# Optimization experiments

Hardware: AMD Instinct MI355X
Metric: run time of the kernel (lower is better)

The kernel has to match this reference:

```python
import jax, jax.numpy as jnp
import numpy as np

N_NODES = 100000
N_REL = 8
IN_FEATS = 64
ATTN_FEATS = 32
NUM_HEADS = 4
N_EDGES = 800000
NEG_SLOPE = 0.2


def setup_inputs() -> dict:
    key = jax.random.key(0)
    ks = jax.random.split(key, 11)
    s = 0.05
    return {
        "feat": jax.random.normal(ks[0], (N_NODES, IN_FEATS), jnp.float32),
        "quality_emb": jax.random.normal(ks[1], (N_NODES, IN_FEATS), jnp.float32),
        "fc_src_w": jax.random.normal(ks[2], (N_REL, IN_FEATS, ATTN_FEATS * NUM_HEADS), jnp.float32) * s,
        "fc_src_b": jax.random.normal(ks[3], (N_REL, ATTN_FEATS * NUM_HEADS), jnp.float32) * s,
        "fc_qual_w": jax.random.normal(ks[4], (N_REL, IN_FEATS, ATTN_FEATS * NUM_HEADS), jnp.float32) * s,
        "fc_qual_b": jax.random.normal(ks[5], (N_REL, ATTN_FEATS * NUM_HEADS), jnp.float32) * s,
        "attn": jax.random.normal(ks[6], (N_REL, NUM_HEADS, ATTN_FEATS), jnp.float32) * s,
        "src": jax.random.randint(ks[7], (N_EDGES,), 0, N_NODES, jnp.int64),
        "dst": jax.random.randint(ks[8], (N_EDGES,), 0, N_NODES, jnp.int64),
        "r_type": jax.random.randint(ks[9], (N_EDGES,), 0, N_REL, jnp.int64),
        "nid": jax.random.randint(ks[10], (N_EDGES,), 0, N_NODES, jnp.int64),
    }


def reference(feat, quality_emb, fc_src_w, fc_src_b, fc_qual_w, fc_qual_b, attn,
              src, dst, r_type, nid):
    # gather_mm(feat[src], fc_src_w, idx_b=r_type) == project per node for all
    # relations (grouped GEMM), then gather [src, r_type] per edge.
    feat_proj = jnp.einsum('ni,rio->nro', feat, fc_src_w)          # [N, R, H*D]
    el = feat_proj[src, r_type] + fc_src_b[r_type]                 # [E, H*D]

    qual_proj = jnp.einsum('ni,rio->nro', quality_emb, fc_qual_w)  # [N, R, H*D]
    qual = qual_proj[nid, r_type] + fc_qual_b[r_type]              # [E, H*D]

    e = jax.nn.leaky_relu((el + qual).reshape(-1, NUM_HEADS, ATTN_FEATS), NEG_SLOPE)
    score = jnp.sum(e * attn[r_type], axis=-1)                     # [E, H]

    # edge softmax grouped by destination node, per head
    m = jax.ops.segment_max(score, dst, num_segments=N_NODES)      # [N, H]
    p = jnp.exp(score - m[dst])
    denom = jax.ops.segment_sum(p, dst, num_segments=N_NODES)      # [N, H]
    a = p / denom[dst]                                             # [E, H]

    # narre: messages use raw source features, weighted by attention
    msg = feat[src][:, None, :] * a[:, :, None]                    # [E, H, IN]
    ft = jax.ops.segment_sum(msg, dst, num_segments=N_NODES)       # [N, H, IN]
    return ft
```

## Files before the change

### kernel.cpp

```cpp
#include <hip/hip_runtime.h>
#include <hip/hip_bf16.h>

#define RELS 8
#define HDD 128
#define NH 4
#define STILES 4
#define MAXDEG 64
#define CAP 104448

typedef __attribute__((ext_vector_type(8))) short bf16x8;
typedef __attribute__((ext_vector_type(4))) float f32x4;
typedef unsigned short u16;

__device__ __forceinline__ u16 f2b(float v){
  union { float f; unsigned u; } x; x.f = v;
  unsigned r = x.u + 0x7fffu + ((x.u >> 16) & 1u);
  return (u16)(r >> 16);
}
__device__ __forceinline__ float b2f(u16 h){
  union { unsigned u; float f; } x; x.u = ((unsigned)h) << 16; return x.f;
}

template<int CTRL>
__device__ __forceinline__ float dpp_mov(float x){
  union { float f; int i; } u; u.f = x;
  u.i = __builtin_amdgcn_update_dpp(0, u.i, CTRL, 0xF, 0xF, false);
  return u.f;
}
__device__ __forceinline__ float row_sum16(float v){
  v += dpp_mov<0x121>(v);
  v += dpp_mov<0x122>(v);
  v += dpp_mov<0x124>(v);
  v += dpp_mov<0x128>(v);
  return v;
}

__global__ void k_prep(const float* __restrict__ wsrc, const float* __restrict__ wqual,
                       const float* __restrict__ bsrc, const float* __restrict__ bqual,
                       u16* __restrict__ Wt, float* __restrict__ biasc,
                       const float* __restrict__ feat, const float* __restrict__ qual,
                       u16* __restrict__ featb, u16* __restrict__ qualb, int total,
                       const int* __restrict__ rt, const int* __restrict__ src,
                       const int* __restrict__ nid, const int* __restrict__ dst,
                       int* __restrict__ rcur, int* __restrict__ deg,
                       int* __restrict__ eIdx,
                       int* __restrict__ srcR, int* __restrict__ nidR, int E,
                       int B2, int B0){
  int b = blockIdx.x, t = threadIdx.x;
  if (b < B2){
    __shared__ int lh[RELS], lb[RELS];
    if (t < RELS) lh[t] = 0;
    __syncthreads();
    int e = b*256 + t;
    int r = 0, rank = 0, sv = 0, nv = 0, dv = 0, rk = 0;
    if (e < E){
      dv = dst[e];
      rk = atomicAdd(&deg[dv], 1);
      sv = src[e]; nv = nid[e];
      r = rt[e];
      rank = atomicAdd(&lh[r], 1);
    }
    __syncthreads();
    if (t < RELS && lh[t] > 0) lb[t] = t*CAP + atomicAdd(&rcur[t], lh[t]);
    __syncthreads();
    if (e < E){
      int pr = lb[r] + rank;
      if (pr < (r+1)*CAP){
        srcR[pr] = sv;
        nidR[pr] = nv;
        if (rk < MAXDEG) eIdx[(size_t)dv*MAXDEG + rk] = pr;
      }
    }
  } else if (b < B2 + B0){
    int g = (b - B2)*256 + t;
    if (g < RELS*HDD*HDD){
      int r = g >> 14, rem = g & 16383, n = rem >> 7, k = rem & 127;
      float v = (k < 64) ? wsrc[r*8192 + k*128 + n] : wqual[r*8192 + (k-64)*128 + n];
      Wt[g] = f2b(v);
    } else {
      int bb = g - RELS*HDD*HDD;
      if (bb < RELS*HDD) biasc[bb] = bsrc[bb] + bqual[bb];
    }
  } else {
    int g = ((b - B2 - B0)*256 + t) * 8;
    const float* sp; u16* dp;
    if (g < total){ sp = feat; dp = featb; }
    else { g -= total; if (g >= total) return; sp = qual; dp = qualb; }
    float4 a = *(const float4*)(sp + g);
    float4 c = *(const float4*)(sp + g + 4);
    union { u16 h[8]; uint4 v; } o;
    o.h[0]=f2b(a.x); o.h[1]=f2b(a.y); o.h[2]=f2b(a.z); o.h[3]=f2b(a.w);
    o.h[4]=f2b(c.x); o.h[5]=f2b(c.y); o.h[6]=f2b(c.z); o.h[7]=f2b(c.w);
    *(uint4*)(dp + g) = o.v;
  }
}

__global__ __launch_bounds__(256) void k_score(
    const u16* __restrict__ featb, const u16* __restrict__ qualb,
    const u16* __restrict__ Wt, const float* __restrict__ biasc,
    const float* __restrict__ attn,
    const int* __restrict__ srcR, const int* __restrict__ nidR,
    const int* __restrict__ rcur,
    float* __restrict__ scoreR){
  __shared__ u16 As[2][64*128];
  int t = threadIdx.x;

  const int NBPR = CAP/256;
  int bid = blockIdx.x;
  int r = bid / NBPR, ch = bid - r*NBPR;
  int cnt_r = min(rcur[r], CAP);
  int base = r*CAP + ch*256;
  int cntR = min(256, cnt_r - ch*256);
  if (cntR <= 0) return;
  int Tact = (cntR + 63) >> 6;

  int mloc = t >> 2, part = t & 3;
  int lane = t & 63, w = t >> 6;
  int lr = lane & 15, lq = lane >> 4;

  const u16* wbase = Wt + r*16384 + (w*32)*128;
  bf16x8 wfrag[2][4];
  #pragma unroll
  for (int mt=0; mt<2; mt++)
    #pragma unroll
    for (int kt=0; kt<4; kt++)
      wfrag[mt][kt] = *(const bf16x8*)(wbase + (mt*16 + lr)*128 + kt*32 + lq*8);

  float attn_p[2][4], attn_n[2][4];
  f32x4 biasv[2];
  #pragma unroll
  for (int mt=0; mt<2; mt++)
    #pragma unroll
    for (int i=0; i<4; i++){
      int c = w*32 + mt*16 + lq*4 + i;
      float a = attn[r*128 + c];
      biasv[mt][i] = biasc[r*128 + c];
      attn_p[mt][i] = a;
      attn_n[mt][i] = 0.2f*a;
    }

  const u16* basep = (part < 2) ? featb : qualb;
  int halfoff = (part & 1)*32;
  int myidx[STILES];
  #pragma unroll
  for (int tt=0; tt<STILES; tt++){
    int eloc = tt*64 + mloc;
    int gi = base + eloc;
    myidx[tt] = (eloc < cntR) ? ((part < 2) ? srcR[gi] : nidR[gi]) : -1;
  }

  uint4 pre[2][4];
  auto fetch = [&](int pb, int idxval){
    if (idxval >= 0){
      const uint4* pv = (const uint4*)(basep + (long long)idxval*64 + halfoff);
      pre[pb][0]=pv[0]; pre[pb][1]=pv[1]; pre[pb][2]=pv[2]; pre[pb][3]=pv[3];
    } else {
      uint4 z = {0,0,0,0};
      pre[pb][0]=z; pre[pb][1]=z; pre[pb][2]=z; pre[pb][3]=z;
    }
  };

  fetch(0, myidx[0]);
  fetch(1, myidx[1]);
  #pragma unroll
  for (int tt=0; tt<STILES; tt++){
    if (tt >= Tact) break;
    const int p = tt & 1;
    uint4* As_v = (uint4*)As[p];
    #pragma unroll
    for (int i=0;i<4;i++){
      int c = part*4 + i;
      As_v[mloc*16 + (c ^ part ^ (mloc & 7))] = pre[p][i];
    }
    if (tt+2 < STILES) fetch(p, myidx[tt+2]);
    asm volatile("s_waitcnt lgkmcnt(0)" ::: "memory");
    __builtin_amdgcn_s_barrier();

    f32x4 acc[4][2];
    #pragma unroll
    for (int et=0; et<4; et++){ acc[et][0]=biasv[0]; acc[et][1]=biasv[1]; }
    #pragma unroll
    for (int et=0; et<4; et++){
      #pragma unroll
      for (int kt=0; kt<4; kt++){
        bf16x8 bf = *(const bf16x8*)&As[p][(et*16 + lr)*128 + (((kt*4 + lq) ^ kt ^ (lr & 7))*8)];
        acc[et][0] = __builtin_amdgcn_mfma_f32_16x16x32_bf16(wfrag[0][kt], bf, acc[et][0], 0, 0, 0);
        acc[et][1] = __builtin_amdgcn_mfma_f32_16x16x32_bf16(wfrag[1][kt], bf, acc[et][1], 0, 0, 0);
      }
    }

    float s0v=0.f, s1v=0.f, s2v=0.f, s3v=0.f;
    #pragma unroll
    for (int mt=0; mt<2; mt++)
      #pragma unroll
      for (int i=0; i<4; i++){
        float x0 = acc[0][mt][i];
        s0v = __builtin_fmaf(fmaxf(x0,0.f), attn_p[mt][i], s0v);
        s0v = __builtin_fmaf(fminf(x0,0.f), attn_n[mt][i], s0v);
        float x1 = acc[1][mt][i];
        s1v = __builtin_fmaf(fmaxf(x1,0.f), attn_p[mt][i], s1v);
        s1v = __builtin_fmaf(fminf(x1,0.f), attn_n[mt][i], s1v);
        float x2 = acc[2][mt][i];
        s2v = __builtin_fmaf(fmaxf(x2,0.f), attn_p[mt][i], s2v);
        s2v = __builtin_fmaf(fminf(x2,0.f), attn_n[mt][i], s2v);
        float x3 = acc[3][mt][i];
        s3v = __builtin_fmaf(fmaxf(x3,0.f), attn_p[mt][i], s3v);
        s3v = __builtin_fmaf(fminf(x3,0.f), attn_n[mt][i], s3v);
      }
    s0v += __shfl_xor(s0v, 16); s0v += __shfl_xor(s0v, 32);
    s1v += __shfl_xor(s1v, 16); s1v += __shfl_xor(s1v, 32);
    s2v += __shfl_xor(s2v, 16); s2v += __shfl_xor(s2v, 32);
    s3v += __shfl_xor(s3v, 16); s3v += __shfl_xor(s3v, 32);
    float v01 = (lq & 1) ? s1v : s0v;
    float v23 = (lq & 1) ? s3v : s2v;
    float v = (lq & 2) ? v23 : v01;
    v = __expf(v);
    int eout = tt*64 + lane;
    if (eout < cntR) scoreR[(size_t)(base + eout)*4 + w] = v;
  }
}

__global__ __launch_bounds__(256) void k_agg(
    const int* __restrict__ deg_a, const int* __restrict__ eIdx,
    const float* __restrict__ scoreR, const int* __restrict__ srcR,
    const u16* __restrict__ featb, float* __restrict__ out, int N){
  __shared__ float ps[4][64][4];
  __shared__ int   ss[4][64];
  int wv = threadIdx.x >> 6, lane = threadIdx.x & 63;
  int node = blockIdx.x*4 + wv;
  if (node >= N) return;
  int deg = min(deg_a[node], MAXDEG);
  float a0=0.f, a1=0.f, a2=0.f, a3=0.f;
  if (deg > 0){
    float d0=0.f,d1=0.f,d2=0.f,d3=0.f;
    float p0=0.f,p1=0.f,p2=0.f,p3=0.f; int sv=0;
    if (lane < deg){
      int pr = eIdx[(size_t)node*MAXDEG + lane];
      float4 sc = *(const float4*)&scoreR[(size_t)pr*4];
      sv = srcR[pr];
      p0=sc.x; p1=sc.y; p2=sc.z; p3=sc.w;
    }
    d0=p0; d1=p1; d2=p2; d3=p3;
    float4 pv = { p0, p1, p2, p3 };
    *(float4*)&ps[wv][lane][0] = pv;
    ss[wv][lane] = sv;
    __builtin_amdgcn_wave_barrier();
    #pragma unroll 4
    for (int e=0; e<deg; e++){
      float4 pe = *(const float4*)&ps[wv][e][0];
      float fv = b2f(featb[(long long)ss[wv][e]*64 + lane]);
      a0 += pe.x*fv; a1 += pe.y*fv; a2 += pe.z*fv; a3 += pe.w*fv;
    }
    __builtin_amdgcn_wave_barrier();
    d0=row_sum16(d0); d1=row_sum16(d1); d2=row_sum16(d2); d3=row_sum16(d3);
    #pragma unroll
    for (int off=16; off<64; off<<=1){
      d0+=__shfl_xor(d0,off); d1+=__shfl_xor(d1,off);
      d2+=__shfl_xor(d2,off); d3+=__shfl_xor(d3,off);
    }
    a0 *= 1.f/d0; a1 *= 1.f/d1; a2 *= 1.f/d2; a3 *= 1.f/d3;
  }
  float* op = out + (long long)node*256;
  op[lane]       = a0;
  op[64 + lane]  = a1;
  op[128 + lane] = a2;
  op[192 + lane] = a3;
}

extern "C" void kernel_launch(void* const* d_in, const int* in_sizes, int n_in,
                              void* d_out, int out_size, void* d_ws, size_t ws_size,
                              hipStream_t stream) {
  const float* feat  = (const float*)d_in[0];
  const float* qual  = (const float*)d_in[1];
  const float* wsrc  = (const float*)d_in[2];
  const float* bsrc  = (const float*)d_in[3];
  const float* wqual = (const float*)d_in[4];
  const float* bqual = (const float*)d_in[5];
  const float* attn  = (const float*)d_in[6];
  const int* src = (const int*)d_in[7];
  const int* dst = (const int*)d_in[8];
  const int* rt  = (const int*)d_in[9];
  const int* nid = (const int*)d_in[10];
  const int E = in_sizes[7];
  const int N = in_sizes[0] / 64;
  float* out = (float*)d_out;

  char* p = (char*)d_ws;
  auto alloc = [&](size_t bytes) -> void* {
    void* q = (void*)p;
    p += (bytes + 255) & ~(size_t)255;
    return q;
  };
  float* scoreR  = (float*)alloc((size_t)RELS*CAP*4*4);
  u16*  featb    = (u16*)  alloc((size_t)N*64*2);
  u16*  qualb    = (u16*)  alloc((size_t)N*64*2);
  u16*  Wt       = (u16*)  alloc((size_t)RELS*HDD*HDD*2);
  float* biasc   = (float*)alloc((size_t)RELS*HDD*4);
  int*  srcR     = (int*)  alloc((size_t)RELS*CAP*4);
  int*  nidR     = (int*)  alloc((size_t)RELS*CAP*4);
  int*  eIdx     = (int*)  alloc((size_t)N*MAXDEG*4);
  char* zbase = p;
  int*  deg      = (int*)  alloc((size_t)N*4);
  int*  rcur     = (int*)  alloc(32);
  size_t zbytes = (size_t)(p - zbase);

  hipMemsetAsync(zbase, 0, zbytes, stream);

  int total = N*64;
  int totw = RELS*HDD*HDD + RELS*HDD;
  int B2 = (E + 255)/256;
  int B0 = (totw + 255)/256;
  int B1 = ((2*total)/8 + 255)/256;
  k_prep<<<B2+B0+B1, 256, 0, stream>>>(wsrc, wqual, bsrc, bqual, Wt, biasc,
                                       feat, qual, featb, qualb, total,
                                       rt, src, nid, dst,
                                       rcur, deg, eIdx, srcR, nidR, E, B2, B0);
  k_score<<<RELS*(CAP/256), 256, 0, stream>>>(featb, qualb, Wt, biasc, attn,
                                              srcR, nidR, rcur, scoreR);
  k_agg<<<(N + 3)/4, 256, 0, stream>>>(deg, eIdx, scoreR, srcR, featb, out, N);
}
```

Baseline: 322.1 us.

## Fuse three kernels into persistent cooperative megakernel with grid syncs

Merges the prep, score and aggregation kernels into a single cooperative persistent kernel that loops over work units and separates the phases with grid-wide syncs. The degree/eIdx scatter moves out of the prep phase into the score phase, running concurrently with the scoring work and going through a new per-edge prOf array. The aim is to remove kernel launch gaps and tail effects between stages. In exchange it adds grid-sync cost, an extra prOf write and read, an occupancy cap from the launch bounds, and the combined LDS footprint of all phases in every block.

```diff
diff --git a/kernel.cpp b/kernel.cpp
--- a/kernel.cpp
+++ b/kernel.cpp
@@ -1,12 +1,14 @@
 #include <hip/hip_runtime.h>
 #include <hip/hip_bf16.h>
+#include <hip/hip_cooperative_groups.h>
+
+namespace cg = cooperative_groups;
 
 #define RELS 8
 #define HDD 128
-#define NH 4
-#define STILES 4
 #define MAXDEG 64
 #define CAP 104448
+#define NBPR (CAP/256)
 
 typedef __attribute__((ext_vector_type(8))) short bf16x8;
 typedef __attribute__((ext_vector_type(4))) float f32x4;
@@ -35,236 +37,253 @@
   return v;
 }
 
-__global__ void k_prep(const float* __restrict__ wsrc, const float* __restrict__ wqual,
-                       const float* __restrict__ bsrc, const float* __restrict__ bqual,
-                       u16* __restrict__ Wt, float* __restrict__ biasc,
-                       const float* __restrict__ feat, const float* __restrict__ qual,
-                       u16* __restrict__ featb, u16* __restrict__ qualb, int total,
-                       const int* __restrict__ rt, const int* __restrict__ src,
-                       const int* __restrict__ nid, const int* __restrict__ dst,
-                       int* __restrict__ rcur, int* __restrict__ deg,
-                       int* __restrict__ eIdx,
-                       int* __restrict__ srcR, int* __restrict__ nidR, int E,
-                       int B2, int B0){
-  int b = blockIdx.x, t = threadIdx.x;
-  if (b < B2){
-    __shared__ int lh[RELS], lb[RELS];
-    if (t < RELS) lh[t] = 0;
-    __syncthreads();
-    int e = b*256 + t;
-    int r = 0, rank = 0, sv = 0, nv = 0, dv = 0, rk = 0;
-    if (e < E){
-      dv = dst[e];
-      rk = atomicAdd(&deg[dv], 1);
-      sv = src[e]; nv = nid[e];
-      r = rt[e];
-      rank = atomicAdd(&lh[r], 1);
-    }
-    __syncthreads();
-    if (t < RELS && lh[t] > 0) lb[t] = t*CAP + atomicAdd(&rcur[t], lh[t]);
-    __syncthreads();
-    if (e < E){
-      int pr = lb[r] + rank;
-      if (pr < (r+1)*CAP){
-        srcR[pr] = sv;
-        nidR[pr] = nv;
-        if (rk < MAXDEG) eIdx[(size_t)dv*MAXDEG + rk] = pr;
-      }
-    }
-  } else if (b < B2 + B0){
-    int g = (b - B2)*256 + t;
-    if (g < RELS*HDD*HDD){
-      int r = g >> 14, rem = g & 16383, n = rem >> 7, k = rem & 127;
-      float v = (k < 64) ? wsrc[r*8192 + k*128 + n] : wqual[r*8192 + (k-64)*128 + n];
-      Wt[g] = f2b(v);
+struct MegaArgs {
+  const float *wsrc, *wqual, *bsrc, *bqual, *feat, *qual, *attn;
+  const int *src, *dst, *rt, *nid;
+  u16 *Wt, *featb, *qualb;
+  float *biasc, *scoreR, *out;
+  int *rcur, *deg, *eIdx, *srcR, *nidR, *prOf;
+  int E, N, total, B2, B0, B1, HU, AU;
+};
+
+__global__ __launch_bounds__(256, 4) void k_mega(MegaArgs a){
+  int t = threadIdx.x;
+  __shared__ int lh[RELS], lb[RELS];
+  __shared__ u16 As[2][64*128];
+  __shared__ float ps[4][64][4];
+  __shared__ int   ss[4][64];
+
+  const int PU = a.B2 + a.B0 + a.B1;
+  for (int u = blockIdx.x; u < PU; u += gridDim.x){
+    if (u < a.B2){
+      if (t < RELS) lh[t] = 0;
+      __syncthreads();
+      int e = u*256 + t;
+      int r = 0, rank = 0, sv = 0, nv = 0;
+      if (e < a.E){
+        sv = a.src[e]; nv = a.nid[e];
+        r = a.rt[e];
+        rank = atomicAdd(&lh[r], 1);
+      }
+      __syncthreads();
+      if (t < RELS && lh[t] > 0) lb[t] = t*CAP + atomicAdd(&a.rcur[t], lh[t]);
+      __syncthreads();
+      if (e < a.E){
+        int pr = lb[r] + rank;
+        if (pr < (r+1)*CAP){
+          a.srcR[pr] = sv;
+          a.nidR[pr] = nv;
+          a.prOf[e] = pr;
+        } else {
+          a.prOf[e] = -1;
+        }
+      }
+    } else if (u < a.B2 + a.B0){
+      int g = (u - a.B2)*256 + t;
+      if (g < RELS*HDD*HDD){
+        int r = g >> 14, rem = g & 16383, n = rem >> 7, k = rem & 127;
+        float v = (k < 64) ? a.wsrc[r*8192 + k*128 + n] : a.wqual[r*8192 + (k-64)*128 + n];
+        a.Wt[g] = f2b(v);
+      } else {
+        int bb = g - RELS*HDD*HDD;
+        if (bb < RELS*HDD) a.biasc[bb] = a.bsrc[bb] + a.bqual[bb];
+      }
     } else {
-      int bb = g - RELS*HDD*HDD;
-      if (bb < RELS*HDD) biasc[bb] = bsrc[bb] + bqual[bb];
-    }
-  } else {
-    int g = ((b - B2 - B0)*256 + t) * 8;
-    const float* sp; u16* dp;
-    if (g < total){ sp = feat; dp = featb; }
-    else { g -= total; if (g >= total) return; sp = qual; dp = qualb; }
-    float4 a = *(const float4*)(sp + g);
-    float4 c = *(const float4*)(sp + g + 4);
-    union { u16 h[8]; uint4 v; } o;
-    o.h[0]=f2b(a.x); o.h[1]=f2b(a.y); o.h[2]=f2b(a.z); o.h[3]=f2b(a.w);
-    o.h[4]=f2b(c.x); o.h[5]=f2b(c.y); o.h[6]=f2b(c.z); o.h[7]=f2b(c.w);
-    *(uint4*)(dp + g) = o.v;
+      int g = ((u - a.B2 - a.B0)*256 + t) * 8;
+      const float* sp = a.feat; u16* dp = a.featb;
+      bool ok = true;
+      if (g >= a.total){
+        g -= a.total;
+        if (g >= a.total) ok = false;
+        else { sp = a.qual; dp = a.qualb; }
+      }
+      if (ok){
+        float4 x = *(const float4*)(sp + g);
+        float4 c = *(const float4*)(sp + g + 4);
+        union { u16 h[8]; uint4 v; } o;
+        o.h[0]=f2b(x.x); o.h[1]=f2b(x.y); o.h[2]=f2b(x.z); o.h[3]=f2b(x.w);
+        o.h[4]=f2b(c.x); o.h[5]=f2b(c.y); o.h[6]=f2b(c.z); o.h[7]=f2b(c.w);
+        *(uint4*)(dp + g) = o.v;
+      }
+    }
   }
-}
-
-__global__ __launch_bounds__(256) void k_score(
-    const u16* __restrict__ featb, const u16* __restrict__ qualb,
-    const u16* __restrict__ Wt, const float* __restrict__ biasc,
-    const float* __restrict__ attn,
-    const int* __restrict__ srcR, const int* __restrict__ nidR,
-    const int* __restrict__ rcur,
-    float* __restrict__ scoreR){
-  __shared__ u16 As[2][64*128];
-  int t = threadIdx.x;
-
-  const int NBPR = CAP/256;
-  int bid = blockIdx.x;
-  int r = bid / NBPR, ch = bid - r*NBPR;
-  int cnt_r = min(rcur[r], CAP);
-  int base = r*CAP + ch*256;
-  int cntR = min(256, cnt_r - ch*256);
-  if (cntR <= 0) return;
-  int Tact = (cntR + 63) >> 6;
+
+  cg::this_grid().sync();
 
   int mloc = t >> 2, part = t & 3;
   int lane = t & 63, w = t >> 6;
   int lr = lane & 15, lq = lane >> 4;
-
-  const u16* wbase = Wt + r*16384 + (w*32)*128;
-  bf16x8 wfrag[2][4];
-  #pragma unroll
-  for (int mt=0; mt<2; mt++)
-    #pragma unroll
-    for (int kt=0; kt<4; kt++)
-      wfrag[mt][kt] = *(const bf16x8*)(wbase + (mt*16 + lr)*128 + kt*32 + lq*8);
-
-  float attn_p[2][4], attn_n[2][4];
-  f32x4 biasv[2];
-  #pragma unroll
-  for (int mt=0; mt<2; mt++)
-    #pragma unroll
-    for (int i=0; i<4; i++){
-      int c = w*32 + mt*16 + lq*4 + i;
-      float a = attn[r*128 + c];
-      biasv[mt][i] = biasc[r*128 + c];
-      attn_p[mt][i] = a;
-      attn_n[mt][i] = 0.2f*a;
-    }
-
-  const u16* basep = (part < 2) ? featb : qualb;
-  int halfoff = (part & 1)*32;
-  int myidx[STILES];
-  #pragma unroll
-  for (int tt=0; tt<STILES; tt++){
-    int eloc = tt*64 + mloc;
-    int gi = base + eloc;
-    myidx[tt] = (eloc < cntR) ? ((part < 2) ? srcR[gi] : nidR[gi]) : -1;
-  }
-
-  uint4 pre[2][4];
-  auto fetch = [&](int pb, int idxval){
-    if (idxval >= 0){
-      const uint4* pv = (const uint4*)(basep + (long long)idxval*64 + halfoff);
-      pre[pb][0]=pv[0]; pre[pb][1]=pv[1]; pre[pb][2]=pv[2]; pre[pb][3]=pv[3];
-    } else {
-      uint4 z = {0,0,0,0};
-      pre[pb][0]=z; pre[pb][1]=z; pre[pb][2]=z; pre[pb][3]=z;
-    }
-  };
-
-  fetch(0, myidx[0]);
-  fetch(1, myidx[1]);
-  #pragma unroll
-  for (int tt=0; tt<STILES; tt++){
-    if (tt >= Tact) break;
-    const int p = tt & 1;
-    uint4* As_v = (uint4*)As[p];
-    #pragma unroll
-    for (int i=0;i<4;i++){
-      int c = part*4 + i;
-      As_v[mloc*16 + (c ^ part ^ (mloc & 7))] = pre[p][i];
-    }
-    if (tt+2 < STILES) fetch(p, myidx[tt+2]);
-    asm volatile("s_waitcnt lgkmcnt(0)" ::: "memory");
-    __builtin_amdgcn_s_barrier();
-
-    f32x4 acc[4][2];
-    #pragma unroll
-    for (int et=0; et<4; et++){ acc[et][0]=biasv[0]; acc[et][1]=biasv[1]; }
-    #pragma unroll
-    for (int et=0; et<4; et++){
-      #pragma unroll
-      for (int kt=0; kt<4; kt++){
-        bf16x8 bf = *(const bf16x8*)&As[p][(et*16 + lr)*128 + (((kt*4 + lq) ^ kt ^ (lr & 7))*8)];
-        acc[et][0] = __builtin_amdgcn_mfma_f32_16x16x32_bf16(wfrag[0][kt], bf, acc[et][0], 0, 0, 0);
-        acc[et][1] = __builtin_amdgcn_mfma_f32_16x16x32_bf16(wfrag[1][kt], bf, acc[et][1], 0, 0, 0);
-      }
-    }
-
-    float s0v=0.f, s1v=0.f, s2v=0.f, s3v=0.f;
+  const int SU = a.HU + RELS*NBPR;
+  for (int u = blockIdx.x; u < SU; u += gridDim.x){
+    if (u < a.HU){
+      int e0 = u*1024 + t;
+      #pragma unroll
+      for (int k4=0; k4<4; k4++){
+        int e = e0 + k4*256;
+        if (e < a.E){
+          int pr = a.prOf[e];
+          if (pr >= 0){
+            int dv = a.dst[e];
+            int rk = atomicAdd(&a.deg[dv], 1);
+            if (rk < MAXDEG) a.eIdx[(size_t)dv*MAXDEG + rk] = pr;
+          }
+        }
+      }
+      continue;
+    }
+    int su = u - a.HU;
+    int r = su / NBPR, ch = su - r*NBPR;
+    int cnt_r = min(a.rcur[r], CAP);
+    int base = r*CAP + ch*256;
+    int cntR = min(256, cnt_r - ch*256);
+    if (cntR <= 0) continue;
+    int Tact = (cntR + 63) >> 6;
+
+    const u16* wbase = a.Wt + r*16384 + (w*32)*128;
+    bf16x8 wfrag[2][4];
     #pragma unroll
     for (int mt=0; mt<2; mt++)
       #pragma unroll
+      for (int kt=0; kt<4; kt++)
+        wfrag[mt][kt] = *(const bf16x8*)(wbase + (mt*16 + lr)*128 + kt*32 + lq*8);
+
+    float attn_p[2][4], attn_n[2][4];
+    f32x4 biasv[2];
+    #pragma unroll
+    for (int mt=0; mt<2; mt++)
+      #pragma unroll
       for (int i=0; i<4; i++){
-        float x0 = acc[0][mt][i];
-        s0v = __builtin_fmaf(fmaxf(x0,0.f), attn_p[mt][i], s0v);
-        s0v = __builtin_fmaf(fminf(x0,0.f), attn_n[mt][i], s0v);
-        float x1 = acc[1][mt][i];
-        s1v = __builtin_fmaf(fmaxf(x1,0.f), attn_p[mt][i], s1v);
-        s1v = __builtin_fmaf(fminf(x1,0.f), attn_n[mt][i], s1v);
-        float x2 = acc[2][mt][i];
-        s2v = __builtin_fmaf(fmaxf(x2,0.f), attn_p[mt][i], s2v);
-        s2v = __builtin_fmaf(fminf(x2,0.f), attn_n[mt][i], s2v);
-        float x3 = acc[3][mt][i];
-        s3v = __builtin_fmaf(fmaxf(x3,0.f), attn_p[mt][i], s3v);
-        s3v = __builtin_fmaf(fminf(x3,0.f), attn_n[mt][i], s3v);
-      }
-    s0v += __shfl_xor(s0v, 16); s0v += __shfl_xor(s0v, 32);
-    s1v += __shfl_xor(s1v, 16); s1v += __shfl_xor(s1v, 32);
-    s2v += __shfl_xor(s2v, 16); s2v += __shfl_xor(s2v, 32);
-    s3v += __shfl_xor(s3v, 16); s3v += __shfl_xor(s3v, 32);
-    float v01 = (lq & 1) ? s1v : s0v;
-    float v23 = (lq & 1) ? s3v : s2v;
-    float v = (lq & 2) ? v23 : v01;
-    v = __expf(v);
-    int eout = tt*64 + lane;
-    if (eout < cntR) scoreR[(size_t)(base + eout)*4 + w] = v;
+        int c = w*32 + mt*16 + lq*4 + i;
+        float av = a.attn[r*128 + c];
+        biasv[mt][i] = a.biasc[r*128 + c];
+        attn_p[mt][i] = av;
+        attn_n[mt][i] = 0.2f*av;
+      }
+
+    const u16* basep = (part < 2) ? a.featb : a.qualb;
+    int halfoff = (part & 1)*32;
+    int myidx[4];
+    #pragma unroll
+    for (int tt=0; tt<4; tt++){
+      int eloc = tt*64 + mloc;
+      int gi = base + eloc;
+      myidx[tt] = (eloc < cntR) ? ((part < 2) ? a.srcR[gi] : a.nidR[gi]) : -1;
+    }
+
+    uint4 pre[2][4];
+    auto fetch = [&](int pb, int idxval){
+      if (idxval >= 0){
+        const uint4* pv = (const uint4*)(basep + (long long)idxval*64 + halfoff);
+        pre[pb][0]=pv[0]; pre[pb][1]=pv[1]; pre[pb][2]=pv[2]; pre[pb][3]=pv[3];
+      } else {
+        uint4 z = {0,0,0,0};
+        pre[pb][0]=z; pre[pb][1]=z; pre[pb][2]=z; pre[pb][3]=z;
+      }
+    };
+
+    fetch(0, myidx[0]);
+    fetch(1, myidx[1]);
+    #pragma unroll
+    for (int tt=0; tt<4; tt++){
+      if (tt >= Tact) break;
+      const int p = tt & 1;
+      uint4* As_v = (uint4*)As[p];
+      #pragma unroll
+      for (int i=0;i<4;i++){
+        int c = part*4 + i;
+        As_v[mloc*16 + (c ^ part ^ (mloc & 7))] = pre[p][i];
+      }
+      if (tt+2 < 4) fetch(p, myidx[tt+2]);
+      asm volatile("s_waitcnt lgkmcnt(0)" ::: "memory");
+      __builtin_amdgcn_s_barrier();
+
+      f32x4 acc[4][2];
+      #pragma unroll
+      for (int et=0; et<4; et++){ acc[et][0]=biasv[0]; acc[et][1]=biasv[1]; }
+      #pragma unroll
+      for (int et=0; et<4; et++){
+        #pragma unroll
+        for (int kt=0; kt<4; kt++){
+          bf16x8 bf = *(const bf16x8*)&As[p][(et*16 + lr)*128 + (((kt*4 + lq) ^ kt ^ (lr & 7))*8)];
+          acc[et][0] = __builtin_amdgcn_mfma_f32_16x16x32_bf16(wfrag[0][kt], bf, acc[et][0], 0, 0, 0);
+          acc[et][1] = __builtin_amdgcn_mfma_f32_16x16x32_bf16(wfrag[1][kt], bf, acc[et][1], 0, 0, 0);
+        }
+      }
+
+      float s0v=0.f, s1v=0.f, s2v=0.f, s3v=0.f;
+      #pragma unroll
+      for (int mt=0; mt<2; mt++)
+        #pragma unroll
+        for (int i=0; i<4; i++){
+          float x0 = acc[0][mt][i];
+          s0v = __builtin_fmaf(fmaxf(x0,0.f), attn_p[mt][i], s0v);
+          s0v = __builtin_fmaf(fminf(x0,0.f), attn_n[mt][i], s0v);
+          float x1 = acc[1][mt][i];
+          s1v = __builtin_fmaf(fmaxf(x1,0.f), attn_p[mt][i], s1v);
+          s1v = __builtin_fmaf(fminf(x1,0.f), attn_n[mt][i], s1v);
+          float x2 = acc[2][mt][i];
+          s2v = __builtin_fmaf(fmaxf(x2,0.f), attn_p[mt][i], s2v);
+          s2v = __builtin_fmaf(fminf(x2,0.f), attn_n[mt][i], s2v);
+          float x3 = acc[3][mt][i];
+          s3v = __builtin_fmaf(fmaxf(x3,0.f), attn_p[mt][i], s3v);
+          s3v = __builtin_fmaf(fminf(x3,0.f), attn_n[mt][i], s3v);
+        }
+      s0v += __shfl_xor(s0v, 16); s0v += __shfl_xor(s0v, 32);
+      s1v += __shfl_xor(s1v, 16); s1v += __shfl_xor(s1v, 32);
+      s2v += __shfl_xor(s2v, 16); s2v += __shfl_xor(s2v, 32);
+      s3v += __shfl_xor(s3v, 16); s3v += __shfl_xor(s3v, 32);
+      float v01 = (lq & 1) ? s1v : s0v;
+      float v23 = (lq & 1) ? s3v : s2v;
+      float v = (lq & 2) ? v23 : v01;
+      v = __expf(v);
+      int eout = tt*64 + lane;
+      if (eout < cntR) a.scoreR[(size_t)(base + eout)*4 + w] = v;
+    }
+    __syncthreads();
   }
-}
-
-__global__ __launch_bounds__(256) void k_agg(
-    const int* __restrict__ deg_a, const int* __restrict__ eIdx,
-    const float* __restrict__ scoreR, const int* __restrict__ srcR,
-    const u16* __restrict__ featb, float* __restrict__ out, int N){
-  __shared__ float ps[4][64][4];
-  __shared__ int   ss[4][64];
-  int wv = threadIdx.x >> 6, lane = threadIdx.x & 63;
-  int node = blockIdx.x*4 + wv;
-  if (node >= N) return;
-  int deg = min(deg_a[node], MAXDEG);
-  float a0=0.f, a1=0.f, a2=0.f, a3=0.f;
-  if (deg > 0){
-    float d0=0.f,d1=0.f,d2=0.f,d3=0.f;
-    float p0=0.f,p1=0.f,p2=0.f,p3=0.f; int sv=0;
-    if (lane < deg){
-      int pr = eIdx[(size_t)node*MAXDEG + lane];
-      float4 sc = *(const float4*)&scoreR[(size_t)pr*4];
-      sv = srcR[pr];
-      p0=sc.x; p1=sc.y; p2=sc.z; p3=sc.w;
-    }
-    d0=p0; d1=p1; d2=p2; d3=p3;
-    float4 pv = { p0, p1, p2, p3 };
-    *(float4*)&ps[wv][lane][0] = pv;
-    ss[wv][lane] = sv;
-    __builtin_amdgcn_wave_barrier();
-    #pragma unroll 4
-    for (int e=0; e<deg; e++){
-      float4 pe = *(const float4*)&ps[wv][e][0];
-      float fv = b2f(featb[(long long)ss[wv][e]*64 + lane]);
-      a0 += pe.x*fv; a1 += pe.y*fv; a2 += pe.z*fv; a3 += pe.w*fv;
-    }
-    __builtin_amdgcn_wave_barrier();
-    d0=row_sum16(d0); d1=row_sum16(d1); d2=row_sum16(d2); d3=row_sum16(d3);
-    #pragma unroll
-    for (int off=16; off<64; off<<=1){
-      d0+=__shfl_xor(d0,off); d1+=__shfl_xor(d1,off);
-      d2+=__shfl_xor(d2,off); d3+=__shfl_xor(d3,off);
-    }
-    a0 *= 1.f/d0; a1 *= 1.f/d1; a2 *= 1.f/d2; a3 *= 1.f/d3;
+
+  cg::this_grid().sync();
+
+  int wv = t >> 6;
+  for (int u = blockIdx.x; u < a.AU; u += gridDim.x){
+    int node = u*4 + wv;
+    if (node >= a.N) continue;
+    int deg = min(a.deg[node], MAXDEG);
+    float* op = a.out + (size_t)node*256;
+    float a0=0.f, a1=0.f, a2=0.f, a3=0.f;
+    if (deg > 0){
+      float p0=0.f,p1=0.f,p2=0.f,p3=0.f; int sv=0;
+      if (lane < deg){
+        int pr = a.eIdx[(size_t)node*MAXDEG + lane];
+        float4 sc = *(const float4*)&a.scoreR[(size_t)pr*4];
+        sv = a.srcR[pr];
+        p0=sc.x; p1=sc.y; p2=sc.z; p3=sc.w;
+      }
+      float d0=p0, d1=p1, d2=p2, d3=p3;
+      float4 pv = { p0, p1, p2, p3 };
+      *(float4*)&ps[wv][lane][0] = pv;
+      ss[wv][lane] = sv;
+      __builtin_amdgcn_wave_barrier();
+      #pragma unroll 4
+      for (int e=0; e<deg; e++){
+        float4 pe = *(const float4*)&ps[wv][e][0];
+        float fv = b2f(a.featb[(long long)ss[wv][e]*64 + lane]);
+        a0 += pe.x*fv; a1 += pe.y*fv; a2 += pe.z*fv; a3 += pe.w*fv;
+      }
+      __builtin_amdgcn_wave_barrier();
+      d0=row_sum16(d0); d1=row_sum16(d1); d2=row_sum16(d2); d3=row_sum16(d3);
+      #pragma unroll
+      for (int off=16; off<64; off<<=1){
+        d0+=__shfl_xor(d0,off); d1+=__shfl_xor(d1,off);
+        d2+=__shfl_xor(d2,off); d3+=__shfl_xor(d3,off);
+      }
+      a0 *= 1.f/d0; a1 *= 1.f/d1; a2 *= 1.f/d2; a3 *= 1.f/d3;
+    }
+    op[lane]       = a0;
+    op[64 + lane]  = a1;
+    op[128 + lane] = a2;
+    op[192 + lane] = a3;
   }
-  float* op = out + (long long)node*256;
-  op[lane]       = a0;
-  op[64 + lane]  = a1;
-  op[128 + lane] = a2;
-  op[192 + lane] = a3;
 }
 
 extern "C" void kernel_launch(void* const* d_in, const int* in_sizes, int n_in,
@@ -298,6 +317,7 @@
   float* biasc   = (float*)alloc((size_t)RELS*HDD*4);
   int*  srcR     = (int*)  alloc((size_t)RELS*CAP*4);
   int*  nidR     = (int*)  alloc((size_t)RELS*CAP*4);
+  int*  prOf     = (int*)  alloc((size_t)E*4);
   int*  eIdx     = (int*)  alloc((size_t)N*MAXDEG*4);
   char* zbase = p;
   int*  deg      = (int*)  alloc((size_t)N*4);
@@ -308,14 +328,28 @@
 
   int total = N*64;
   int totw = RELS*HDD*HDD + RELS*HDD;
-  int B2 = (E + 255)/256;
-  int B0 = (totw + 255)/256;
-  int B1 = ((2*total)/8 + 255)/256;
-  k_prep<<<B2+B0+B1, 256, 0, stream>>>(wsrc, wqual, bsrc, bqual, Wt, biasc,
-                                       feat, qual, featb, qualb, total,
-                                       rt, src, nid, dst,
-                                       rcur, deg, eIdx, srcR, nidR, E, B2, B0);
-  k_score<<<RELS*(CAP/256), 256, 0, stream>>>(featb, qualb, Wt, biasc, attn,
-                                              srcR, nidR, rcur, scoreR);
-  k_agg<<<(N + 3)/4, 256, 0, stream>>>(deg, eIdx, scoreR, srcR, featb, out, N);
-}
+  MegaArgs a;
+  a.wsrc = wsrc; a.wqual = wqual; a.bsrc = bsrc; a.bqual = bqual;
+  a.feat = feat; a.qual = qual; a.attn = attn;
+  a.src = src; a.dst = dst; a.rt = rt; a.nid = nid;
+  a.Wt = Wt; a.featb = featb; a.qualb = qualb;
+  a.biasc = biasc; a.scoreR = scoreR; a.out = out;
+  a.rcur = rcur; a.deg = deg; a.eIdx = eIdx;
+  a.srcR = srcR; a.nidR = nidR; a.prOf = prOf;
+  a.E = E; a.N = N; a.total = total;
+  a.B2 = (E + 255)/256;
+  a.B0 = (totw + 255)/256;
+  a.B1 = ((2*total)/8 + 255)/256;
+  a.HU = (E + 1023)/1024;
+  a.AU = (N + 3)/4;
+
+  int maxb = 4;
+  hipOccupancyMaxActiveBlocksPerMultiprocessor(&maxb, k_mega, 256, 0);
+  if (maxb < 1) maxb = 1;
+  if (maxb > 8) maxb = 8;
+  int grid = maxb * 256;
+
+  void* kargs[] = { (void*)&a };
+  hipLaunchCooperativeKernel((const void*)k_mega, dim3(grid), dim3(256),
+                             kargs, 0, stream);
+}
```

Measured after the change: 717.9 us. 123% more time.

## Move degree histogram and CSR index build into score kernel blocks

Applied to the files above, without the earlier changes.

The per-destination degree atomics and the eIdx writes move out of the prep kernel. Prep now records dst in relation-sorted order (dstR), and 256 extra blocks at the start of the score kernel scan dstR to build deg and eIdx while the GEMM blocks compute scores. This takes the dependent atomic and scatter off the prep critical path and overlaps it with score computation. In exchange it adds an extra dstR write and read, and eIdx now fills in relation-sorted order, so edges past MAXDEG are dropped in a different order.

```diff
diff --git a/kernel.cpp b/kernel.cpp
--- a/kernel.cpp
+++ b/kernel.cpp
@@ -3,10 +3,11 @@
 
 #define RELS 8
 #define HDD 128
-#define NH 4
 #define STILES 4
 #define MAXDEG 64
 #define CAP 104448
+#define NBPR (CAP/256)
+#define BHIST 256
 
 typedef __attribute__((ext_vector_type(8))) short bf16x8;
 typedef __attribute__((ext_vector_type(4))) float f32x4;
@@ -42,9 +43,9 @@
                        u16* __restrict__ featb, u16* __restrict__ qualb, int total,
                        const int* __restrict__ rt, const int* __restrict__ src,
                        const int* __restrict__ nid, const int* __restrict__ dst,
-                       int* __restrict__ rcur, int* __restrict__ deg,
-                       int* __restrict__ eIdx,
-                       int* __restrict__ srcR, int* __restrict__ nidR, int E,
+                       int* __restrict__ rcur,
+                       int* __restrict__ srcR, int* __restrict__ nidR,
+                       int* __restrict__ dstR, int E,
                        int B2, int B0){
   int b = blockIdx.x, t = threadIdx.x;
   if (b < B2){
@@ -52,11 +53,9 @@
     if (t < RELS) lh[t] = 0;
     __syncthreads();
     int e = b*256 + t;
-    int r = 0, rank = 0, sv = 0, nv = 0, dv = 0, rk = 0;
+    int r = 0, rank = 0, sv = 0, nv = 0, dv = 0;
     if (e < E){
-      dv = dst[e];
-      rk = atomicAdd(&deg[dv], 1);
-      sv = src[e]; nv = nid[e];
+      sv = src[e]; nv = nid[e]; dv = dst[e];
       r = rt[e];
       rank = atomicAdd(&lh[r], 1);
     }
@@ -68,7 +67,7 @@
       if (pr < (r+1)*CAP){
         srcR[pr] = sv;
         nidR[pr] = nv;
-        if (rk < MAXDEG) eIdx[(size_t)dv*MAXDEG + rk] = pr;
+        dstR[pr] = dv;
       }
     }
   } else if (b < B2 + B0){
@@ -100,13 +99,29 @@
     const u16* __restrict__ Wt, const float* __restrict__ biasc,
     const float* __restrict__ attn,
     const int* __restrict__ srcR, const int* __restrict__ nidR,
-    const int* __restrict__ rcur,
+    const int* __restrict__ dstR, const int* __restrict__ rcur,
+    int* __restrict__ deg, int* __restrict__ eIdx,
     float* __restrict__ scoreR){
   __shared__ u16 As[2][64*128];
   int t = threadIdx.x;
-
-  const int NBPR = CAP/256;
-  int bid = blockIdx.x;
+  int b = blockIdx.x;
+
+  if (b < BHIST){
+    #pragma unroll
+    for (int rr=0; rr<RELS; rr++){
+      int cnt_r = min(rcur[rr], CAP);
+      int base_r = rr*CAP;
+      for (int i = b*256 + t; i < cnt_r; i += BHIST*256){
+        int pr = base_r + i;
+        int dv = dstR[pr];
+        int rk = atomicAdd(&deg[dv], 1);
+        if (rk < MAXDEG) eIdx[(size_t)dv*MAXDEG + rk] = pr;
+      }
+    }
+    return;
+  }
+
+  int bid = b - BHIST;
   int r = bid / NBPR, ch = bid - r*NBPR;
   int cnt_r = min(rcur[r], CAP);
   int base = r*CAP + ch*256;
@@ -232,7 +247,6 @@
   int deg = min(deg_a[node], MAXDEG);
   float a0=0.f, a1=0.f, a2=0.f, a3=0.f;
   if (deg > 0){
-    float d0=0.f,d1=0.f,d2=0.f,d3=0.f;
     float p0=0.f,p1=0.f,p2=0.f,p3=0.f; int sv=0;
     if (lane < deg){
       int pr = eIdx[(size_t)node*MAXDEG + lane];
@@ -240,7 +254,7 @@
       sv = srcR[pr];
       p0=sc.x; p1=sc.y; p2=sc.z; p3=sc.w;
     }
-    d0=p0; d1=p1; d2=p2; d3=p3;
+    float d0=p0, d1=p1, d2=p2, d3=p3;
     float4 pv = { p0, p1, p2, p3 };
     *(float4*)&ps[wv][lane][0] = pv;
     ss[wv][lane] = sv;
@@ -298,6 +312,7 @@
   float* biasc   = (float*)alloc((size_t)RELS*HDD*4);
   int*  srcR     = (int*)  alloc((size_t)RELS*CAP*4);
   int*  nidR     = (int*)  alloc((size_t)RELS*CAP*4);
+  int*  dstR     = (int*)  alloc((size_t)RELS*CAP*4);
   int*  eIdx     = (int*)  alloc((size_t)N*MAXDEG*4);
   char* zbase = p;
   int*  deg      = (int*)  alloc((size_t)N*4);
@@ -314,8 +329,9 @@
   k_prep<<<B2+B0+B1, 256, 0, stream>>>(wsrc, wqual, bsrc, bqual, Wt, biasc,
                                        feat, qual, featb, qualb, total,
                                        rt, src, nid, dst,
-                                       rcur, deg, eIdx, srcR, nidR, E, B2, B0);
-  k_score<<<RELS*(CAP/256), 256, 0, stream>>>(featb, qualb, Wt, biasc, attn,
-                                              srcR, nidR, rcur, scoreR);
+                                       rcur, srcR, nidR, dstR, E, B2, B0);
+  k_score<<<BHIST + RELS*NBPR, 256, 0, stream>>>(featb, qualb, Wt, biasc, attn,
+                                                 srcR, nidR, dstR, rcur,
+                                                 deg, eIdx, scoreR);
   k_agg<<<(N + 3)/4, 256, 0, stream>>>(deg, eIdx, scoreR, srcR, featb, out, N);
 }
```

Measured after the change: 329.0 us. 2.1% more time.
